# Kernel tuning notes

Measured on AMD Instinct MI355X. Metric: run time of the kernel, lower is better.

The kernel has to match this reference:

```python
import jax, jax.numpy as jnp
import numpy as np

B, S, H, R, N = 8, 4096, 1024, 128, 256
A_LOGIT_INIT = 6.906754778648554      # logit(0.999)
DELTA_LOG_INIT = 0.5413248546129181   # log(exp(1.0) - 1.0), softplus^-1(1.0)


def setup_inputs() -> dict:
    key = jax.random.key(0)
    ks = jax.random.split(key, 6)
    x = jax.random.normal(ks[0], (B, S, H), dtype=jnp.float32)
    state0 = jnp.zeros((B, N), dtype=jnp.float32)
    in_basis = jax.random.normal(ks[1], (R, H), dtype=jnp.float32) / np.sqrt(H)
    q_select = jax.random.normal(ks[2], (N, R), dtype=jnp.float32) / np.sqrt(R)
    k_select = jax.random.normal(ks[3], (N, R), dtype=jnp.float32) / np.sqrt(R)
    v_input = jax.random.normal(ks[4], (N, R), dtype=jnp.float32) / np.sqrt(R)
    out_proj = jax.random.normal(ks[5], (H, N), dtype=jnp.float32) / np.sqrt(N)
    a_logit = jnp.full((N,), A_LOGIT_INIT, dtype=jnp.float32)
    delta_log = jnp.full((N,), DELTA_LOG_INIT, dtype=jnp.float32)
    return {"x": x, "state0": state0, "in_basis": in_basis, "q_select": q_select,
            "k_select": k_select, "v_input": v_input, "out_proj": out_proj,
            "a_logit": a_logit, "delta_log": delta_log}


def reference(x, state0, in_basis, q_select, k_select, v_input, out_proj,
              a_logit, delta_log):
    # Projections (all timesteps at once; equivalent to per-step F.linear)
    z = jnp.einsum('bsh,rh->bsr', x, in_basis)          # [B,S,R]
    b = jnp.einsum('bsr,nr->bsn', z, k_select)          # [B,S,N]
    c = jnp.einsum('bsr,nr->bsn', z, q_select)          # [B,S,N]
    v = jnp.einsum('bsr,nr->bsn', z, v_input)           # [B,S,N]

    a = jax.nn.sigmoid(a_logit)                         # [N]
    delta = jax.nn.softplus(delta_log)                  # [N]
    u = delta * (b * v)                                 # [B,S,N] driving input

    # Diagonal linear recurrence: s_t = a * s_{t-1} + u_t ; y_t = c_t * s_t
    u_t = jnp.swapaxes(u, 0, 1)                         # [S,B,N]
    c_t = jnp.swapaxes(c, 0, 1)                         # [S,B,N]

    def step(s, inp):
        u_i, c_i = inp
        s = a * s + u_i
        return s, c_i * s

    final_state, ys = jax.lax.scan(step, state0, (u_t, c_t))  # ys: [S,B,N]
    out = jnp.einsum('sbn,hn->bsh', ys, out_proj)       # [B,S,H]
    return out, final_state
```

## Files before the change

kernel.cpp:

```cpp
#include <hip/hip_runtime.h>
#include <math.h>

#define Bb 8
#define Ss 4096
#define Hh 1024
#define Rr 128
#define Nn 256
#define Mm (Bb*Ss)
#define LCH 128
#define NCHK (Ss/LCH)

typedef __attribute__((ext_vector_type(8))) short bf16x8;
typedef __attribute__((ext_vector_type(4))) float f32x4;

__device__ __forceinline__ float sigmoidf_(float x) { return 1.0f / (1.0f + expf(-x)); }
__device__ __forceinline__ float softplusf_(float x) { return log1pf(expf(x)); }

__device__ __forceinline__ unsigned short f2b(float f) {
    union { float f; unsigned int u; } v; v.f = f;
    return (unsigned short)((v.u + 0x7fffu + ((v.u >> 16) & 1u)) >> 16);
}
__device__ __forceinline__ float b2f(unsigned short h) {
    union { unsigned int u; float f; } v; v.u = ((unsigned int)h) << 16;
    return v.f;
}

__device__ __forceinline__ void gl_lds16(const void* g, void* l) {
    __builtin_amdgcn_global_load_lds(
        (const __attribute__((address_space(1))) void*)g,
        (__attribute__((address_space(3))) void*)l, 16, 0, 0);
}

__global__ __launch_bounds__(256)
void cast_x(const float* __restrict__ src, unsigned short* __restrict__ dst)
{
    const size_t i = ((size_t)blockIdx.x * 256 + threadIdx.x) * 8;
    const float4 a = *(const float4*)(src + i);
    const float4 b = *(const float4*)(src + i + 4);
    uint4 o;
    o.x = (unsigned)f2b(a.x) | ((unsigned)f2b(a.y) << 16);
    o.y = (unsigned)f2b(a.z) | ((unsigned)f2b(a.w) << 16);
    o.z = (unsigned)f2b(b.x) | ((unsigned)f2b(b.y) << 16);
    o.w = (unsigned)f2b(b.z) | ((unsigned)f2b(b.w) << 16);
    *(uint4*)(dst + i) = o;
}

__global__ __launch_bounds__(256)
void cast_w(const float* __restrict__ s0, const float* __restrict__ s1,
            const float* __restrict__ s2, const float* __restrict__ s3,
            const float* __restrict__ s4,
            unsigned short* __restrict__ d0, unsigned short* __restrict__ d1,
            unsigned short* __restrict__ d2, unsigned short* __restrict__ d3,
            unsigned short* __restrict__ d4)
{
    const int i = blockIdx.x * 256 + threadIdx.x;
    if (i < 131072)      d0[i] = f2b(s0[i]);
    else if (i < 163840) d1[i - 131072] = f2b(s1[i - 131072]);
    else if (i < 196608) d2[i - 163840] = f2b(s2[i - 163840]);
    else if (i < 229376) d3[i - 196608] = f2b(s3[i - 196608]);
    else                 d4[i - 229376] = f2b(s4[i - 229376]);
}

template <bool OUT_BF16>
__global__ __launch_bounds__(256)
void mfma_nt(const unsigned short* __restrict__ A, const unsigned short* __restrict__ B,
             void* __restrict__ Cout, int M, int N, int K)
{
    __shared__ __align__(16) unsigned short As[128 * 32];
    __shared__ __align__(16) unsigned short Bs[128 * 32];
    const int tid = threadIdx.x;
    const int wave = tid >> 6, lane = tid & 63;
    const int m0 = blockIdx.x * 128, n0 = blockIdx.y * 128;
    const int wm = (wave & 1) * 64, wn = (wave >> 1) * 64;
    const int quad = lane >> 4, lm = lane & 15;
    const int srow = lane >> 2;
    const int skoff = (lane & 3) * 8;
    const int r0 = wave * 2, r1 = r0 + 1;

    f32x4 acc[4][4] = {};

    for (int k0 = 0; k0 < K; k0 += 32) {
        gl_lds16(A + (size_t)(m0 + r0 * 16 + srow) * K + k0 + skoff, &As[r0 * 512]);
        gl_lds16(A + (size_t)(m0 + r1 * 16 + srow) * K + k0 + skoff, &As[r1 * 512]);
        gl_lds16(B + (size_t)(n0 + r0 * 16 + srow) * K + k0 + skoff, &Bs[r0 * 512]);
        gl_lds16(B + (size_t)(n0 + r1 * 16 + srow) * K + k0 + skoff, &Bs[r1 * 512]);
        __syncthreads();
        bf16x8 af[4], bfv[4];
#pragma unroll
        for (int i = 0; i < 4; ++i)
            af[i] = *(const bf16x8*)&As[(wm + i * 16 + lm) * 32 + quad * 8];
#pragma unroll
        for (int j = 0; j < 4; ++j)
            bfv[j] = *(const bf16x8*)&Bs[(wn + j * 16 + lm) * 32 + quad * 8];
#pragma unroll
        for (int i = 0; i < 4; ++i)
#pragma unroll
            for (int j = 0; j < 4; ++j)
                acc[i][j] = __builtin_amdgcn_mfma_f32_16x16x32_bf16(af[i], bfv[j], acc[i][j], 0, 0, 0);
        __syncthreads();
    }

#pragma unroll
    for (int i = 0; i < 4; ++i) {
        const int rbase = m0 + wm + i * 16 + quad * 4;
#pragma unroll
        for (int j = 0; j < 4; ++j) {
            const int col = n0 + wn + j * 16 + lm;
#pragma unroll
            for (int r = 0; r < 4; ++r) {
                if (OUT_BF16)
                    ((unsigned short*)Cout)[(size_t)(rbase + r) * N + col] = f2b(acc[i][j][r]);
                else
                    ((float*)Cout)[(size_t)(rbase + r) * N + col] = acc[i][j][r];
            }
        }
    }
}

__global__ __launch_bounds__(256)
void proj_mfma(const unsigned short* __restrict__ Z, const unsigned short* __restrict__ Kw,
               const unsigned short* __restrict__ Qw, const unsigned short* __restrict__ Vw,
               const float* __restrict__ delta_log,
               unsigned short* __restrict__ U, unsigned short* __restrict__ C)
{
    __shared__ __align__(16) unsigned short zs[128 * 32];
    __shared__ __align__(16) unsigned short ks[128 * 32];
    __shared__ __align__(16) unsigned short qs[128 * 32];
    __shared__ __align__(16) unsigned short vs[128 * 32];
    const int tid = threadIdx.x;
    const int wave = tid >> 6, lane = tid & 63;
    const int m0 = blockIdx.x * 128, n0 = blockIdx.y * 128;
    const int wm = (wave & 1) * 64, wn = (wave >> 1) * 64;
    const int quad = lane >> 4, lm = lane & 15;
    const int srow = lane >> 2;
    const int skoff = (lane & 3) * 8;
    const int r0 = wave * 2, r1 = r0 + 1;

    f32x4 aB[4][4] = {}, aC[4][4] = {}, aV[4][4] = {};

    for (int k0 = 0; k0 < Rr; k0 += 32) {
        gl_lds16(Z  + (size_t)(m0 + r0 * 16 + srow) * Rr + k0 + skoff, &zs[r0 * 512]);
        gl_lds16(Z  + (size_t)(m0 + r1 * 16 + srow) * Rr + k0 + skoff, &zs[r1 * 512]);
        gl_lds16(Kw + (size_t)(n0 + r0 * 16 + srow) * Rr + k0 + skoff, &ks[r0 * 512]);
        gl_lds16(Kw + (size_t)(n0 + r1 * 16 + srow) * Rr + k0 + skoff, &ks[r1 * 512]);
        gl_lds16(Qw + (size_t)(n0 + r0 * 16 + srow) * Rr + k0 + skoff, &qs[r0 * 512]);
        gl_lds16(Qw + (size_t)(n0 + r1 * 16 + srow) * Rr + k0 + skoff, &qs[r1 * 512]);
        gl_lds16(Vw + (size_t)(n0 + r0 * 16 + srow) * Rr + k0 + skoff, &vs[r0 * 512]);
        gl_lds16(Vw + (size_t)(n0 + r1 * 16 + srow) * Rr + k0 + skoff, &vs[r1 * 512]);
        __syncthreads();
        bf16x8 zf[4], wf[4];
#pragma unroll
        for (int i = 0; i < 4; ++i)
            zf[i] = *(const bf16x8*)&zs[(wm + i * 16 + lm) * 32 + quad * 8];
#pragma unroll
        for (int j = 0; j < 4; ++j)
            wf[j] = *(const bf16x8*)&ks[(wn + j * 16 + lm) * 32 + quad * 8];
#pragma unroll
        for (int i = 0; i < 4; ++i)
#pragma unroll
            for (int j = 0; j < 4; ++j)
                aB[i][j] = __builtin_amdgcn_mfma_f32_16x16x32_bf16(zf[i], wf[j], aB[i][j], 0, 0, 0);
#pragma unroll
        for (int j = 0; j < 4; ++j)
            wf[j] = *(const bf16x8*)&qs[(wn + j * 16 + lm) * 32 + quad * 8];
#pragma unroll
        for (int i = 0; i < 4; ++i)
#pragma unroll
            for (int j = 0; j < 4; ++j)
                aC[i][j] = __builtin_amdgcn_mfma_f32_16x16x32_bf16(zf[i], wf[j], aC[i][j], 0, 0, 0);
#pragma unroll
        for (int j = 0; j < 4; ++j)
            wf[j] = *(const bf16x8*)&vs[(wn + j * 16 + lm) * 32 + quad * 8];
#pragma unroll
        for (int i = 0; i < 4; ++i)
#pragma unroll
            for (int j = 0; j < 4; ++j)
                aV[i][j] = __builtin_amdgcn_mfma_f32_16x16x32_bf16(zf[i], wf[j], aV[i][j], 0, 0, 0);
        __syncthreads();
    }

    float dl[4];
#pragma unroll
    for (int j = 0; j < 4; ++j)
        dl[j] = softplusf_(delta_log[n0 + wn + j * 16 + lm]);

#pragma unroll
    for (int i = 0; i < 4; ++i) {
        const int rbase = m0 + wm + i * 16 + quad * 4;
#pragma unroll
        for (int j = 0; j < 4; ++j) {
            const int col = n0 + wn + j * 16 + lm;
#pragma unroll
            for (int r = 0; r < 4; ++r) {
                const size_t idx = (size_t)(rbase + r) * Nn + col;
                U[idx] = f2b(dl[j] * aB[i][j][r] * aV[i][j][r]);
                C[idx] = f2b(aC[i][j][r]);
            }
        }
    }
}

__global__ __launch_bounds__(256)
void scan_chunk_a(const unsigned short* __restrict__ u, const float* __restrict__ a_logit,
                  float* __restrict__ P)
{
    const int g = blockIdx.x * blockDim.x + threadIdx.x;
    const int n = g & (Nn - 1);
    const int rest = g >> 8;
    const int ch = rest & (NCHK - 1);
    const int b = rest >> 5;
    const float a = sigmoidf_(a_logit[n]);
    const unsigned short* p = u + ((size_t)(b * Ss + ch * LCH)) * Nn + n;
    float s = 0.0f;
#pragma unroll 8
    for (int t = 0; t < LCH; ++t) {
        s = fmaf(a, s, b2f(*p));
        p += Nn;
    }
    P[((size_t)(b * NCHK + ch)) * Nn + n] = s;
}

__global__ __launch_bounds__(256)
void scan_mid(const float* __restrict__ P, const float* __restrict__ state0,
              const float* __restrict__ a_logit,
              float* __restrict__ start, float* __restrict__ final_state)
{
    const int g = blockIdx.x * blockDim.x + threadIdx.x;
    const int n = g & (Nn - 1);
    const int b = g >> 8;
    const float a = sigmoidf_(a_logit[n]);
    float aL = a;
#pragma unroll
    for (int i = 0; i < 7; ++i) aL *= aL;
    float s = state0[g];
    for (int ch = 0; ch < NCHK; ++ch) {
        const size_t idx = ((size_t)(b * NCHK + ch)) * Nn + n;
        start[idx] = s;
        s = fmaf(aL, s, P[idx]);
    }
    final_state[g] = s;
}

__global__ __launch_bounds__(256)
void scan_chunk_c(unsigned short* __restrict__ uy, const unsigned short* __restrict__ cm,
                  const float* __restrict__ start, const float* __restrict__ a_logit)
{
    const int g = blockIdx.x * blockDim.x + threadIdx.x;
    const int n = g & (Nn - 1);
    const int rest = g >> 8;
    const int ch = rest & (NCHK - 1);
    const int b = rest >> 5;
    const float a = sigmoidf_(a_logit[n]);
    float s = start[((size_t)(b * NCHK + ch)) * Nn + n];
    size_t idx = ((size_t)(b * Ss + ch * LCH)) * Nn + n;
#pragma unroll 8
    for (int t = 0; t < LCH; ++t) {
        s = fmaf(a, s, b2f(uy[idx]));
        uy[idx] = f2b(b2f(cm[idx]) * s);
        idx += Nn;
    }
}

extern "C" void kernel_launch(void* const* d_in, const int* in_sizes, int n_in,
                              void* d_out, int out_size, void* d_ws, size_t ws_size,
                              hipStream_t stream)
{
    const float* x         = (const float*)d_in[0];
    const float* state0    = (const float*)d_in[1];
    const float* in_basis  = (const float*)d_in[2];
    const float* q_select  = (const float*)d_in[3];
    const float* k_select  = (const float*)d_in[4];
    const float* v_input   = (const float*)d_in[5];
    const float* out_proj  = (const float*)d_in[6];
    const float* a_logit   = (const float*)d_in[7];
    const float* delta_log = (const float*)d_in[8];

    float* out = (float*)d_out;
    float* final_state = out + (size_t)Mm * Hh;

    char* ws = (char*)d_ws;
    unsigned short* xb = (unsigned short*)ws;
    unsigned short* u  = (unsigned short*)ws;
    unsigned short* c  = (unsigned short*)(ws + 16777216);
    unsigned short* zb = (unsigned short*)(ws + 67108864);
    unsigned short* ib = (unsigned short*)(ws + 75497472);
    unsigned short* kb = (unsigned short*)(ws + 75497472 + 262144);
    unsigned short* qb = (unsigned short*)(ws + 75497472 + 327680);
    unsigned short* vb = (unsigned short*)(ws + 75497472 + 393216);
    unsigned short* ob = (unsigned short*)(ws + 75497472 + 458752);
    float* P  = (float*)(ws + 76480512);
    float* st = (float*)(ws + 76742656);

    cast_x<<<Mm * Hh / (256 * 8), 256, 0, stream>>>(x, xb);
    cast_w<<<491520 / 256, 256, 0, stream>>>(in_basis, k_select, q_select, v_input, out_proj,
                                             ib, kb, qb, vb, ob);

    mfma_nt<true><<<dim3(Mm / 128, Rr / 128), 256, 0, stream>>>(xb, ib, zb, Mm, Rr, Hh);

    proj_mfma<<<dim3(Mm / 128, Nn / 128), 256, 0, stream>>>(zb, kb, qb, vb, delta_log, u, c);

    scan_chunk_a<<<(Bb * NCHK * Nn) / 256, 256, 0, stream>>>(u, a_logit, P);
    scan_mid<<<(Bb * Nn) / 256, 256, 0, stream>>>(P, state0, a_logit, st, final_state);
    scan_chunk_c<<<(Bb * NCHK * Nn) / 256, 256, 0, stream>>>(u, c, st, a_logit);

    mfma_nt<false><<<dim3(Mm / 128, Hh / 128), 256, 0, stream>>>(u, ob, out, Mm, Hh, Nn);
}
```

Before: 350.6 us.

## Fuse x cast into first GEMM and chunk-sum scan into projection kernel

Removes the separate fp32-to-bf16 cast pass over x by converting x tiles to bf16 while staging them into LDS inside the first GEMM, which now uses 64-row tiles. Also folds the per-chunk partial scan (scan_chunk_a) into the projection kernel epilogue: each block keeps its u tile in LDS, computes 32-step local scans per segment, and combines them into the chunk carry. This avoids writing and re-reading the bf16 x copy and an extra pass over u. The cost is synchronous fp32 global loads in the GEMM instead of async direct-to-LDS loads, smaller tiles, and more LDS and epilogue work in the projection kernel.

```diff
diff --git a/kernel.cpp b/kernel.cpp
--- a/kernel.cpp
+++ b/kernel.cpp
@@ -32,20 +32,6 @@
 }
 
 __global__ __launch_bounds__(256)
-void cast_x(const float* __restrict__ src, unsigned short* __restrict__ dst)
-{
-    const size_t i = ((size_t)blockIdx.x * 256 + threadIdx.x) * 8;
-    const float4 a = *(const float4*)(src + i);
-    const float4 b = *(const float4*)(src + i + 4);
-    uint4 o;
-    o.x = (unsigned)f2b(a.x) | ((unsigned)f2b(a.y) << 16);
-    o.y = (unsigned)f2b(a.z) | ((unsigned)f2b(a.w) << 16);
-    o.z = (unsigned)f2b(b.x) | ((unsigned)f2b(b.y) << 16);
-    o.w = (unsigned)f2b(b.z) | ((unsigned)f2b(b.w) << 16);
-    *(uint4*)(dst + i) = o;
-}
-
-__global__ __launch_bounds__(256)
 void cast_w(const float* __restrict__ s0, const float* __restrict__ s1,
             const float* __restrict__ s2, const float* __restrict__ s3,
             const float* __restrict__ s4,
@@ -61,39 +47,46 @@
     else                 d4[i - 229376] = f2b(s4[i - 229376]);
 }
 
-template <bool OUT_BF16>
-__global__ __launch_bounds__(256)
-void mfma_nt(const unsigned short* __restrict__ A, const unsigned short* __restrict__ B,
-             void* __restrict__ Cout, int M, int N, int K)
-{
-    __shared__ __align__(16) unsigned short As[128 * 32];
+__global__ __launch_bounds__(256)
+void g1_fused(const float* __restrict__ X, const unsigned short* __restrict__ IB,
+              unsigned short* __restrict__ Z)
+{
+    __shared__ __align__(16) unsigned short As[64 * 32];
     __shared__ __align__(16) unsigned short Bs[128 * 32];
     const int tid = threadIdx.x;
     const int wave = tid >> 6, lane = tid & 63;
-    const int m0 = blockIdx.x * 128, n0 = blockIdx.y * 128;
-    const int wm = (wave & 1) * 64, wn = (wave >> 1) * 64;
+    const int m0 = blockIdx.x * 64;
+    const int wm = (wave & 1) * 32, wn = (wave >> 1) * 64;
     const int quad = lane >> 4, lm = lane & 15;
     const int srow = lane >> 2;
     const int skoff = (lane & 3) * 8;
-    const int r0 = wave * 2, r1 = r0 + 1;
-
-    f32x4 acc[4][4] = {};
-
-    for (int k0 = 0; k0 < K; k0 += 32) {
-        gl_lds16(A + (size_t)(m0 + r0 * 16 + srow) * K + k0 + skoff, &As[r0 * 512]);
-        gl_lds16(A + (size_t)(m0 + r1 * 16 + srow) * K + k0 + skoff, &As[r1 * 512]);
-        gl_lds16(B + (size_t)(n0 + r0 * 16 + srow) * K + k0 + skoff, &Bs[r0 * 512]);
-        gl_lds16(B + (size_t)(n0 + r1 * 16 + srow) * K + k0 + skoff, &Bs[r1 * 512]);
-        __syncthreads();
-        bf16x8 af[4], bfv[4];
-#pragma unroll
-        for (int i = 0; i < 4; ++i)
+    const int arow = tid >> 3;
+    const int akf = (tid & 7) * 4;
+
+    f32x4 acc[2][4] = {};
+
+    for (int k0 = 0; k0 < Hh; k0 += 32) {
+#pragma unroll
+        for (int q = 0; q < 2; ++q) {
+            const int row = q * 32 + arow;
+            const float4 v = *(const float4*)(X + (size_t)(m0 + row) * Hh + k0 + akf);
+            uint2 o;
+            o.x = (unsigned)f2b(v.x) | ((unsigned)f2b(v.y) << 16);
+            o.y = (unsigned)f2b(v.z) | ((unsigned)f2b(v.w) << 16);
+            *(uint2*)&As[row * 32 + akf] = o;
+        }
+        gl_lds16(IB + (size_t)(2 * wave * 16 + srow) * Hh + k0 + skoff, &Bs[wave * 1024]);
+        gl_lds16(IB + (size_t)((2 * wave + 1) * 16 + srow) * Hh + k0 + skoff, &Bs[wave * 1024 + 512]);
+        __syncthreads();
+        bf16x8 af[2], bfv[4];
+#pragma unroll
+        for (int i = 0; i < 2; ++i)
             af[i] = *(const bf16x8*)&As[(wm + i * 16 + lm) * 32 + quad * 8];
 #pragma unroll
         for (int j = 0; j < 4; ++j)
             bfv[j] = *(const bf16x8*)&Bs[(wn + j * 16 + lm) * 32 + quad * 8];
 #pragma unroll
-        for (int i = 0; i < 4; ++i)
+        for (int i = 0; i < 2; ++i)
 #pragma unroll
             for (int j = 0; j < 4; ++j)
                 acc[i][j] = __builtin_amdgcn_mfma_f32_16x16x32_bf16(af[i], bfv[j], acc[i][j], 0, 0, 0);
@@ -101,123 +94,122 @@
     }
 
 #pragma unroll
-    for (int i = 0; i < 4; ++i) {
+    for (int i = 0; i < 2; ++i) {
         const int rbase = m0 + wm + i * 16 + quad * 4;
 #pragma unroll
         for (int j = 0; j < 4; ++j) {
-            const int col = n0 + wn + j * 16 + lm;
-#pragma unroll
-            for (int r = 0; r < 4; ++r) {
-                if (OUT_BF16)
-                    ((unsigned short*)Cout)[(size_t)(rbase + r) * N + col] = f2b(acc[i][j][r]);
-                else
-                    ((float*)Cout)[(size_t)(rbase + r) * N + col] = acc[i][j][r];
-            }
+            const int col = wn + j * 16 + lm;
+#pragma unroll
+            for (int r = 0; r < 4; ++r)
+                Z[(size_t)(rbase + r) * Rr + col] = f2b(acc[i][j][r]);
         }
     }
 }
 
 __global__ __launch_bounds__(256)
-void proj_mfma(const unsigned short* __restrict__ Z, const unsigned short* __restrict__ Kw,
+void proj_mfma(const unsigned short* __restrict__ Zm, const unsigned short* __restrict__ Kw,
                const unsigned short* __restrict__ Qw, const unsigned short* __restrict__ Vw,
-               const float* __restrict__ delta_log,
-               unsigned short* __restrict__ U, unsigned short* __restrict__ C)
-{
-    __shared__ __align__(16) unsigned short zs[128 * 32];
-    __shared__ __align__(16) unsigned short ks[128 * 32];
-    __shared__ __align__(16) unsigned short qs[128 * 32];
-    __shared__ __align__(16) unsigned short vs[128 * 32];
+               const float* __restrict__ delta_log, const float* __restrict__ a_logit,
+               unsigned short* __restrict__ U, unsigned short* __restrict__ C,
+               float* __restrict__ Pout)
+{
+    __shared__ __align__(16) char smem[34816];
+    unsigned short* zs = (unsigned short*)smem;
+    unsigned short* ks = (unsigned short*)(smem + 8192);
+    unsigned short* qs = (unsigned short*)(smem + 12288);
+    unsigned short* vs = (unsigned short*)(smem + 16384);
+    float* uL = (float*)smem;
+    float* pcomb = (float*)(smem + 33792);
+
     const int tid = threadIdx.x;
     const int wave = tid >> 6, lane = tid & 63;
-    const int m0 = blockIdx.x * 128, n0 = blockIdx.y * 128;
-    const int wm = (wave & 1) * 64, wn = (wave >> 1) * 64;
+    const int m0 = blockIdx.x * 128, n0 = blockIdx.y * 64;
+    const int wm = (wave & 1) * 64, wn = (wave >> 1) * 32;
     const int quad = lane >> 4, lm = lane & 15;
     const int srow = lane >> 2;
     const int skoff = (lane & 3) * 8;
-    const int r0 = wave * 2, r1 = r0 + 1;
-
-    f32x4 aB[4][4] = {}, aC[4][4] = {}, aV[4][4] = {};
+
+    f32x4 aB[4][2] = {}, aC[4][2] = {}, aV[4][2] = {};
 
     for (int k0 = 0; k0 < Rr; k0 += 32) {
-        gl_lds16(Z  + (size_t)(m0 + r0 * 16 + srow) * Rr + k0 + skoff, &zs[r0 * 512]);
-        gl_lds16(Z  + (size_t)(m0 + r1 * 16 + srow) * Rr + k0 + skoff, &zs[r1 * 512]);
-        gl_lds16(Kw + (size_t)(n0 + r0 * 16 + srow) * Rr + k0 + skoff, &ks[r0 * 512]);
-        gl_lds16(Kw + (size_t)(n0 + r1 * 16 + srow) * Rr + k0 + skoff, &ks[r1 * 512]);
-        gl_lds16(Qw + (size_t)(n0 + r0 * 16 + srow) * Rr + k0 + skoff, &qs[r0 * 512]);
-        gl_lds16(Qw + (size_t)(n0 + r1 * 16 + srow) * Rr + k0 + skoff, &qs[r1 * 512]);
-        gl_lds16(Vw + (size_t)(n0 + r0 * 16 + srow) * Rr + k0 + skoff, &vs[r0 * 512]);
-        gl_lds16(Vw + (size_t)(n0 + r1 * 16 + srow) * Rr + k0 + skoff, &vs[r1 * 512]);
-        __syncthreads();
-        bf16x8 zf[4], wf[4];
+        gl_lds16(Zm + (size_t)(m0 + 2 * wave * 16 + srow) * Rr + k0 + skoff, &zs[wave * 1024]);
+        gl_lds16(Zm + (size_t)(m0 + (2 * wave + 1) * 16 + srow) * Rr + k0 + skoff, &zs[wave * 1024 + 512]);
+        gl_lds16(Kw + (size_t)(n0 + wave * 16 + srow) * Rr + k0 + skoff, &ks[wave * 512]);
+        gl_lds16(Qw + (size_t)(n0 + wave * 16 + srow) * Rr + k0 + skoff, &qs[wave * 512]);
+        gl_lds16(Vw + (size_t)(n0 + wave * 16 + srow) * Rr + k0 + skoff, &vs[wave * 512]);
+        __syncthreads();
+        bf16x8 zf[4], wf[2];
 #pragma unroll
         for (int i = 0; i < 4; ++i)
             zf[i] = *(const bf16x8*)&zs[(wm + i * 16 + lm) * 32 + quad * 8];
 #pragma unroll
-        for (int j = 0; j < 4; ++j)
+        for (int j = 0; j < 2; ++j)
             wf[j] = *(const bf16x8*)&ks[(wn + j * 16 + lm) * 32 + quad * 8];
 #pragma unroll
         for (int i = 0; i < 4; ++i)
 #pragma unroll
-            for (int j = 0; j < 4; ++j)
+            for (int j = 0; j < 2; ++j)
                 aB[i][j] = __builtin_amdgcn_mfma_f32_16x16x32_bf16(zf[i], wf[j], aB[i][j], 0, 0, 0);
 #pragma unroll
-        for (int j = 0; j < 4; ++j)
+        for (int j = 0; j < 2; ++j)
             wf[j] = *(const bf16x8*)&qs[(wn + j * 16 + lm) * 32 + quad * 8];
 #pragma unroll
         for (int i = 0; i < 4; ++i)
 #pragma unroll
-            for (int j = 0; j < 4; ++j)
+            for (int j = 0; j < 2; ++j)
                 aC[i][j] = __builtin_amdgcn_mfma_f32_16x16x32_bf16(zf[i], wf[j], aC[i][j], 0, 0, 0);
 #pragma unroll
-        for (int j = 0; j < 4; ++j)
+        for (int j = 0; j < 2; ++j)
             wf[j] = *(const bf16x8*)&vs[(wn + j * 16 + lm) * 32 + quad * 8];
 #pragma unroll
         for (int i = 0; i < 4; ++i)
 #pragma unroll
-            for (int j = 0; j < 4; ++j)
+            for (int j = 0; j < 2; ++j)
                 aV[i][j] = __builtin_amdgcn_mfma_f32_16x16x32_bf16(zf[i], wf[j], aV[i][j], 0, 0, 0);
         __syncthreads();
     }
 
-    float dl[4];
-#pragma unroll
-    for (int j = 0; j < 4; ++j)
+    float dl[2];
+#pragma unroll
+    for (int j = 0; j < 2; ++j)
         dl[j] = softplusf_(delta_log[n0 + wn + j * 16 + lm]);
 
 #pragma unroll
     for (int i = 0; i < 4; ++i) {
-        const int rbase = m0 + wm + i * 16 + quad * 4;
-#pragma unroll
-        for (int j = 0; j < 4; ++j) {
-            const int col = n0 + wn + j * 16 + lm;
+        const int lrow = wm + i * 16 + quad * 4;
+        const int rbase = m0 + lrow;
+#pragma unroll
+        for (int j = 0; j < 2; ++j) {
+            const int col = wn + j * 16 + lm;
+            const int gcol = n0 + col;
 #pragma unroll
             for (int r = 0; r < 4; ++r) {
-                const size_t idx = (size_t)(rbase + r) * Nn + col;
-                U[idx] = f2b(dl[j] * aB[i][j][r] * aV[i][j][r]);
+                const float uval = dl[j] * aB[i][j][r] * aV[i][j][r];
+                const size_t idx = (size_t)(rbase + r) * Nn + gcol;
+                U[idx] = f2b(uval);
                 C[idx] = f2b(aC[i][j][r]);
+                uL[(lrow + r) * 66 + col] = uval;
             }
         }
     }
-}
-
-__global__ __launch_bounds__(256)
-void scan_chunk_a(const unsigned short* __restrict__ u, const float* __restrict__ a_logit,
-                  float* __restrict__ P)
-{
-    const int g = blockIdx.x * blockDim.x + threadIdx.x;
-    const int n = g & (Nn - 1);
-    const int rest = g >> 8;
-    const int ch = rest & (NCHK - 1);
-    const int b = rest >> 5;
-    const float a = sigmoidf_(a_logit[n]);
-    const unsigned short* p = u + ((size_t)(b * Ss + ch * LCH)) * Nn + n;
-    float s = 0.0f;
+    __syncthreads();
+
+    const int colp = tid & 63, seg = tid >> 6;
+    const float a = sigmoidf_(a_logit[n0 + colp]);
+    float l = 0.0f;
 #pragma unroll 8
-    for (int t = 0; t < LCH; ++t) {
-        s = fmaf(a, s, b2f(*p));
-        p += Nn;
-    }
-    P[((size_t)(b * NCHK + ch)) * Nn + n] = s;
+    for (int r = 0; r < 32; ++r)
+        l = fmaf(a, l, uL[(seg * 32 + r) * 66 + colp]);
+    pcomb[seg * 64 + colp] = l;
+    __syncthreads();
+    if (tid < 64) {
+        float a32 = a;
+#pragma unroll
+        for (int i = 0; i < 5; ++i) a32 *= a32;
+        const float Pv = ((pcomb[tid] * a32 + pcomb[64 + tid]) * a32
+                          + pcomb[128 + tid]) * a32 + pcomb[192 + tid];
+        Pout[(size_t)blockIdx.x * Nn + n0 + tid] = Pv;
+    }
 }
 
 __global__ __launch_bounds__(256)
@@ -233,6 +225,7 @@
 #pragma unroll
     for (int i = 0; i < 7; ++i) aL *= aL;
     float s = state0[g];
+#pragma unroll
     for (int ch = 0; ch < NCHK; ++ch) {
         const size_t idx = ((size_t)(b * NCHK + ch)) * Nn + n;
         start[idx] = s;
@@ -261,6 +254,57 @@
     }
 }
 
+__global__ __launch_bounds__(256)
+void mfma_nt_f32(const unsigned short* __restrict__ A, const unsigned short* __restrict__ B,
+                 float* __restrict__ Cout, int M, int N, int K)
+{
+    __shared__ __align__(16) unsigned short As[128 * 32];
+    __shared__ __align__(16) unsigned short Bs[128 * 32];
+    const int tid = threadIdx.x;
+    const int wave = tid >> 6, lane = tid & 63;
+    const int m0 = blockIdx.x * 128, n0 = blockIdx.y * 128;
+    const int wm = (wave & 1) * 64, wn = (wave >> 1) * 64;
+    const int quad = lane >> 4, lm = lane & 15;
+    const int srow = lane >> 2;
+    const int skoff = (lane & 3) * 8;
+    const int r0 = wave * 2, r1 = r0 + 1;
+
+    f32x4 acc[4][4] = {};
+
+    for (int k0 = 0; k0 < K; k0 += 32) {
+        gl_lds16(A + (size_t)(m0 + r0 * 16 + srow) * K + k0 + skoff, &As[r0 * 512]);
+        gl_lds16(A + (size_t)(m0 + r1 * 16 + srow) * K + k0 + skoff, &As[r1 * 512]);
+        gl_lds16(B + (size_t)(n0 + r0 * 16 + srow) * K + k0 + skoff, &Bs[r0 * 512]);
+        gl_lds16(B + (size_t)(n0 + r1 * 16 + srow) * K + k0 + skoff, &Bs[r1 * 512]);
+        __syncthreads();
+        bf16x8 af[4], bfv[4];
+#pragma unroll
+        for (int i = 0; i < 4; ++i)
+            af[i] = *(const bf16x8*)&As[(wm + i * 16 + lm) * 32 + quad * 8];
+#pragma unroll
+        for (int j = 0; j < 4; ++j)
+            bfv[j] = *(const bf16x8*)&Bs[(wn + j * 16 + lm) * 32 + quad * 8];
+#pragma unroll
+        for (int i = 0; i < 4; ++i)
+#pragma unroll
+            for (int j = 0; j < 4; ++j)
+                acc[i][j] = __builtin_amdgcn_mfma_f32_16x16x32_bf16(af[i], bfv[j], acc[i][j], 0, 0, 0);
+        __syncthreads();
+    }
+
+#pragma unroll
+    for (int i = 0; i < 4; ++i) {
+        const int rbase = m0 + wm + i * 16 + quad * 4;
+#pragma unroll
+        for (int j = 0; j < 4; ++j) {
+            const int col = n0 + wn + j * 16 + lm;
+#pragma unroll
+            for (int r = 0; r < 4; ++r)
+                Cout[(size_t)(rbase + r) * N + col] = acc[i][j][r];
+        }
+    }
+}
+
 extern "C" void kernel_launch(void* const* d_in, const int* in_sizes, int n_in,
                               void* d_out, int out_size, void* d_ws, size_t ws_size,
                               hipStream_t stream)
@@ -279,29 +323,27 @@
     float* final_state = out + (size_t)Mm * Hh;
 
     char* ws = (char*)d_ws;
-    unsigned short* xb = (unsigned short*)ws;
     unsigned short* u  = (unsigned short*)ws;
     unsigned short* c  = (unsigned short*)(ws + 16777216);
-    unsigned short* zb = (unsigned short*)(ws + 67108864);
-    unsigned short* ib = (unsigned short*)(ws + 75497472);
-    unsigned short* kb = (unsigned short*)(ws + 75497472 + 262144);
-    unsigned short* qb = (unsigned short*)(ws + 75497472 + 327680);
-    unsigned short* vb = (unsigned short*)(ws + 75497472 + 393216);
-    unsigned short* ob = (unsigned short*)(ws + 75497472 + 458752);
-    float* P  = (float*)(ws + 76480512);
-    float* st = (float*)(ws + 76742656);
-
-    cast_x<<<Mm * Hh / (256 * 8), 256, 0, stream>>>(x, xb);
+    unsigned short* zb = (unsigned short*)(ws + 33554432);
+    unsigned short* ib = (unsigned short*)(ws + 41943040);
+    unsigned short* kb = (unsigned short*)(ws + 42205184);
+    unsigned short* qb = (unsigned short*)(ws + 42270720);
+    unsigned short* vb = (unsigned short*)(ws + 42336256);
+    unsigned short* ob = (unsigned short*)(ws + 42401792);
+    float* P  = (float*)(ws + 42926080);
+    float* st = (float*)(ws + 43188224);
+
     cast_w<<<491520 / 256, 256, 0, stream>>>(in_basis, k_select, q_select, v_input, out_proj,
                                              ib, kb, qb, vb, ob);
 
-    mfma_nt<true><<<dim3(Mm / 128, Rr / 128), 256, 0, stream>>>(xb, ib, zb, Mm, Rr, Hh);
-
-    proj_mfma<<<dim3(Mm / 128, Nn / 128), 256, 0, stream>>>(zb, kb, qb, vb, delta_log, u, c);
-
-    scan_chunk_a<<<(Bb * NCHK * Nn) / 256, 256, 0, stream>>>(u, a_logit, P);
+    g1_fused<<<Mm / 64, 256, 0, stream>>>(x, ib, zb);
+
+    proj_mfma<<<dim3(Mm / 128, Nn / 64), 256, 0, stream>>>(zb, kb, qb, vb,
+                                                           delta_log, a_logit, u, c, P);
+
     scan_mid<<<(Bb * Nn) / 256, 256, 0, stream>>>(P, state0, a_logit, st, final_state);
     scan_chunk_c<<<(Bb * NCHK * Nn) / 256, 256, 0, stream>>>(u, c, st, a_logit);
 
-    mfma_nt<false><<<dim3(Mm / 128, Hh / 128), 256, 0, stream>>>(u, ob, out, Mm, Hh, Nn);
-}
+    mfma_nt_f32<<<dim3(Mm / 128, Hh / 128), 256, 0, stream>>>(u, ob, out, Mm, Hh, Nn);
+}
```

Result: faster. 325.6 us (-7.1%).
